# Kernel optimization log

Measured on AMD Instinct MI355X. Metric: run time of the kernel, lower is better.

## Reference

```python
import jax, jax.numpy as jnp
import numpy as np

NEG = -1e30  # log-space -inf surrogate (safe for logaddexp in fp32)


def _ctc_mean_loss(y_true, y_pred):
    """tf.nn.ctc_loss with blank_index=-1, logit_length=T, label_length=#nonzero.

    y_true: [B, L] int labels, 0 = padding, packed at the front.
    y_pred: [B, T, C] logits. blank = C-1. Returns mean NLL over batch.
    """
    B, L = y_true.shape
    T, C = y_pred.shape[1], y_pred.shape[2]
    blank = C - 1
    S = 2 * L + 1  # extended label length (blanks interleaved)

    label_length = jnp.sum((y_true != 0).astype(jnp.int32), axis=1)  # [B]
    logp = jax.nn.log_softmax(y_pred, axis=-1)  # [B, T, C]

    # Extended sequence: blank, l1, blank, l2, ..., blank
    ext = jnp.full((B, S), blank, dtype=jnp.int32)
    ext = ext.at[:, 1::2].set(y_true.astype(jnp.int32))  # [B, S]

    # skip transition (s-2 -> s) allowed only at odd s>=3 when labels differ
    skip_ok = jnp.zeros((B, S), dtype=bool)
    skip_ok = skip_ok.at[:, 3::2].set(y_true[:, 1:] != y_true[:, :-1])

    # alpha_0
    alpha0 = jnp.full((B, S), NEG, dtype=logp.dtype)
    alpha0 = alpha0.at[:, 0].set(logp[:, 0, blank])
    alpha0 = alpha0.at[:, 1].set(
        jnp.take_along_axis(logp[:, 0, :], ext[:, 1:2], axis=1)[:, 0])

    def step(alpha, logp_t):  # alpha [B,S], logp_t [B,C]
        s1 = jnp.pad(alpha, ((0, 0), (1, 0)), constant_values=NEG)[:, :-1]
        s2 = jnp.pad(alpha, ((0, 0), (2, 0)), constant_values=NEG)[:, :-2]
        comb = jnp.logaddexp(jnp.logaddexp(alpha, s1),
                             jnp.where(skip_ok, s2, NEG))
        emit = jnp.take_along_axis(logp_t, ext, axis=1)  # [B,S]
        return comb + emit, None

    alphaT, _ = jax.lax.scan(step, alpha0, jnp.swapaxes(logp, 0, 1)[1:])

    # P(labels) = alpha_T[2l] + alpha_T[2l-1]  (last blank / last label)
    l = label_length
    idx = jnp.stack([2 * l, 2 * l - 1], axis=1)  # [B,2], l>=1 by construction
    fin = jnp.take_along_axis(alphaT, idx, axis=1)
    loss = -jnp.logaddexp(fin[:, 0], fin[:, 1])  # [B]
    return jnp.mean(loss)


def setup_inputs() -> dict:
    key = jax.random.key(0)
    k1, k2, k3 = jax.random.split(key, 3)
    B, T, L, C = 256, 512, 128, 128
    lengths = jax.random.randint(k1, (B,), L // 2, L + 1)  # labels per example
    vals = jax.random.randint(k2, (B, L), 1, C - 1)  # classes 1..C-2 (blank=C-1)
    mask = jnp.arange(L)[None, :] < lengths[:, None]
    y_true = jnp.where(mask, vals, 0).astype(jnp.int32)
    y_pred = jax.random.normal(k3, (B, T, C), dtype=jnp.float32)
    return {"y_true": y_true, "y_pred": y_pred}


def reference(y_true, y_pred):
    return _ctc_mean_loss(y_true, y_pred)
```

## Files before the change

kernel.cpp:

```cpp
#include <hip/hip_runtime.h>
#include <hip/hip_fp16.h>

#define LN2D 0.6931471805599453094172321

typedef float v2f __attribute__((ext_vector_type(2)));

__device__ __forceinline__ float shr1(float v, float fill) {
    return __int_as_float(__builtin_amdgcn_update_dpp(
        __float_as_int(fill), __float_as_int(v), 0x138 , 0xF, 0xF, false));
}
__device__ __forceinline__ float shl1(float v, float fill) {
    return __int_as_float(__builtin_amdgcn_update_dpp(
        __float_as_int(fill), __float_as_int(v), 0x130 , 0xF, 0xF, false));
}

__device__ __forceinline__ float wave_sum63(float x) {
    int t;
    t = __builtin_amdgcn_update_dpp(0, __float_as_int(x), 0x111, 0xF, 0xF, true);
    x += __int_as_float(t);
    t = __builtin_amdgcn_update_dpp(0, __float_as_int(x), 0x112, 0xF, 0xF, true);
    x += __int_as_float(t);
    t = __builtin_amdgcn_update_dpp(0, __float_as_int(x), 0x114, 0xF, 0xF, true);
    x += __int_as_float(t);
    t = __builtin_amdgcn_update_dpp(0, __float_as_int(x), 0x118, 0xF, 0xF, true);
    x += __int_as_float(t);
    t = __builtin_amdgcn_update_dpp(0, __float_as_int(x), 0x142, 0xA, 0xF, true);
    x += __int_as_float(t);
    t = __builtin_amdgcn_update_dpp(0, __float_as_int(x), 0x143, 0xC, 0xF, true);
    x += __int_as_float(t);
    return x;
}

__device__ __forceinline__ float wave_max63(float x) {
    int iv = __float_as_int(x); int t;
    t = __builtin_amdgcn_update_dpp(iv, iv, 0x111, 0xF, 0xF, false);
    x = fmaxf(x, __int_as_float(t)); iv = __float_as_int(x);
    t = __builtin_amdgcn_update_dpp(iv, iv, 0x112, 0xF, 0xF, false);
    x = fmaxf(x, __int_as_float(t)); iv = __float_as_int(x);
    t = __builtin_amdgcn_update_dpp(iv, iv, 0x114, 0xF, 0xF, false);
    x = fmaxf(x, __int_as_float(t)); iv = __float_as_int(x);
    t = __builtin_amdgcn_update_dpp(iv, iv, 0x118, 0xF, 0xF, false);
    x = fmaxf(x, __int_as_float(t)); iv = __float_as_int(x);
    t = __builtin_amdgcn_update_dpp(iv, iv, 0x142, 0xA, 0xF, false);
    x = fmaxf(x, __int_as_float(t)); iv = __float_as_int(x);
    t = __builtin_amdgcn_update_dpp(iv, iv, 0x143, 0xC, 0xF, false);
    x = fmaxf(x, __int_as_float(t));
    return x;
}

__device__ __forceinline__ float rdl63(float v) {
    return __int_as_float(__builtin_amdgcn_readlane(__float_as_int(v), 63));
}

__device__ __forceinline__ int pk_bf16(float a, float b) {
    unsigned ua = __float_as_uint(a), ub = __float_as_uint(b);
    ua = (ua + 0x7FFFu + ((ua >> 16) & 1u)) >> 16;
    ub = (ub + 0x7FFFu + ((ub >> 16) & 1u)) & 0xFFFF0000u;
    return (int)(ua | ub);
}

#define VSTRIDE 260

__global__ __launch_bounds__(256) void ctc_half(const int* __restrict__ yt,
                                                const float* __restrict__ yp,
                                                float* __restrict__ V,
                                                int* __restrict__ E,
                                                float* __restrict__ accW) {
    constexpr int L = 128;
    const int bh   = blockIdx.x;
    const int b    = bh >> 1, h = bh & 1;
    const int w    = threadIdx.x >> 6;
    const int lane = threadIdx.x & 63;

    __shared__ int g[256][64];

    const int2 cc = *reinterpret_cast<const int2*>(yt + b * L + 2 * lane);
    const int c1 = cc.x, c3 = cc.y;
    const int sl1 = c1 >> 1, sh1v = (c1 & 1) << 4;
    const int sl3 = c3 >> 1, sh3v = (c3 & 1) << 4;

    float acc = 0.0f;
    const float* src = yp + ((size_t)b * 512 + h * 256 + w * 64) * 128 + lane * 2;
    v2f A8[8], B8[8];

#define ISSUE8(d_, p_)                                                         \
    asm volatile(                                                              \
        "global_load_dwordx2 %0, %8, off\n\t"                                  \
        "global_load_dwordx2 %1, %8, off offset:512\n\t"                       \
        "global_load_dwordx2 %2, %8, off offset:1024\n\t"                      \
        "global_load_dwordx2 %3, %8, off offset:1536\n\t"                      \
        "global_load_dwordx2 %4, %8, off offset:2048\n\t"                      \
        "global_load_dwordx2 %5, %8, off offset:2560\n\t"                      \
        "global_load_dwordx2 %6, %8, off offset:3072\n\t"                      \
        "global_load_dwordx2 %7, %8, off offset:3584"                          \
        : "=&v"(d_[0]), "=&v"(d_[1]), "=&v"(d_[2]), "=&v"(d_[3]),              \
          "=&v"(d_[4]), "=&v"(d_[5]), "=&v"(d_[6]), "=&v"(d_[7])               \
        : "v"(p_)                                                              \
        : "memory");

#define WAITN(n_)                                                              \
    {                                                                          \
        asm volatile("s_waitcnt vmcnt(" #n_ ")" ::: "memory");                 \
        __builtin_amdgcn_sched_barrier(0);                                     \
    }

#define PROC8(buf_, rb_)                                                       \
    {                                                                          \
        _Pragma("unroll")                                                      \
        for (int i = 0; i < 8; ++i) {                                          \
            const float vx = buf_[i].x, vy = buf_[i].y;                        \
            const float sall = rdl63(wave_sum63(__expf(vx) + __expf(vy)));     \
            const float xbv  = rdl63(vy);                \
            acc += __logf(sall) - xbv;                                         \
            const __half2 hh = __floats2half2_rn(vx, vy);                      \
            const int hb = __builtin_bit_cast(int, hh);                        \
            const int q1 = __shfl(hb, sl1, 64);                                \
            const int q3 = __shfl(hb, sl3, 64);                                \
            const float x1 = __half2float(__builtin_bit_cast(__half, (unsigned short)(q1 >> sh1v))); \
            const float x3 = __half2float(__builtin_bit_cast(__half, (unsigned short)(q3 >> sh3v))); \
            g[w * 64 + (rb_) + i][lane] =                                      \
                pk_bf16(__expf(x1 - xbv), __expf(x3 - xbv));                   \
        }                                                                      \
    }

    ISSUE8(A8, src)
    ISSUE8(B8, src + 8 * 128)
    WAITN(8)  PROC8(A8, 0)   ISSUE8(A8, src + 16 * 128)
    WAITN(8)  PROC8(B8, 8)   ISSUE8(B8, src + 24 * 128)
    WAITN(8)  PROC8(A8, 16)  ISSUE8(A8, src + 32 * 128)
    WAITN(8)  PROC8(B8, 24)  ISSUE8(B8, src + 40 * 128)
    WAITN(8)  PROC8(A8, 32)  ISSUE8(A8, src + 48 * 128)
    WAITN(8)  PROC8(B8, 40)  ISSUE8(B8, src + 56 * 128)
    WAITN(8)  PROC8(A8, 48)
    WAITN(0)  PROC8(B8, 56)

    if (lane == 0) accW[bh * 4 + w] = acc;
    __syncthreads();

    if (w == 0) {
        const int cprev = __shfl_up(c3, 1, 64);
        const float sk1 = (lane > 0 && c1 != cprev) ? 1.0f : 0.0f;
        const float sk3 = (c3 != c1) ? 1.0f : 0.0f;
        const float skB3 = shl1(sk1, 0.0f);
        const int llen = __popcll(__ballot(c1 != 0)) + __popcll(__ballot(c3 != 0));

        float o0, o1, o2, o3, o4;
        int   Eacc = 0;
        int   er[8];

#define RENORM()                                                               \
    {                                                                          \
        float mr = fmaxf(fmaxf(fmaxf(o0, o1), fmaxf(o2, o3)), o4);             \
        const float mru = rdl63(wave_max63(mr));                               \
        const int ie = (__float_as_int(mru) >> 23) & 0xFF;                     \
        const float sc = __int_as_float((253 - ie) << 23);                     \
        o0 *= sc; o1 *= sc; o2 *= sc; o3 *= sc; o4 *= sc;                      \
        Eacc += ie - 126;                                                      \
    }

#define FSTEP(bits_, rn_)                                                      \
    {                                                                          \
        const float e1 = __int_as_float((bits_) << 16);                        \
        const float e3 = __int_as_float((bits_) & 0xFFFF0000);                 \
        const float pm = shr1(o3, 0.0f);                                       \
        const float n0 = o0 + pm;                                              \
        const float n1 = (o1 + o0 + sk1 * pm) * e1;                            \
        const float n2 = o2 + o1;                                              \
        const float n3 = (o3 + o2 + sk3 * o1) * e3;                            \
        o4 += o3;                                                              \
        o0 = n0; o1 = n1; o2 = n2; o3 = n3;                                    \
        if (rn_) RENORM();                                                     \
    }

#define BSTEP(bits_, rn_)                                                      \
    {                                                                          \
        const float e1 = __int_as_float((bits_) << 16);                        \
        const float e3 = __int_as_float((bits_) & 0xFFFF0000);                 \
        const float g1 = o1 * e1;                                              \
        const float g3 = o3 * e3;                                              \
        const float pm0 = shl1(o0, o4);          \
        const float pm1 = shl1(g1, 0.0f);        \
        const float n0 = o0 + g1;                                              \
        const float n1 = g1 + o2 + sk3 * g3;                                   \
        const float n2 = o2 + g3;                                              \
        const float n3 = g3 + pm0 + skB3 * pm1;                                \
        o0 = n0; o1 = n1; o2 = n2; o3 = n3;                                    \
        if (rn_) RENORM();                                                     \
    }

        if (h == 0) {
            #pragma unroll
            for (int i = 0; i < 8; ++i) er[i] = g[i][lane];
            {
                const float e10 = __int_as_float(er[0] << 16);
                o0 = (lane == 0) ? 1.0f : 0.0f;
                o1 = (lane == 0) ? e10 : 0.0f;
                o2 = 0.0f; o3 = 0.0f; o4 = 0.0f;
            }
            er[0] = g[8][lane];
            #pragma unroll
            for (int t = 1; t < 8; ++t) { FSTEP(er[t], false); er[t] = g[t + 8][lane]; }
            #pragma unroll
            for (int tb = 8; tb < 248; tb += 8) {
                #pragma unroll
                for (int j = 0; j < 8; ++j) {
                    FSTEP(er[j], ((tb + j) & 31) == 0);
                    er[j] = g[tb + j + 8][lane];
                }
            }
            #pragma unroll
            for (int t = 248; t < 256; ++t) FSTEP(er[t & 7], false);
        } else {
            #pragma unroll
            for (int i = 0; i < 8; ++i) er[i] = g[255 - i][lane];
            const int sA = 2 * llen, sB = 2 * llen - 1;
            o0 = (4 * lane + 0 == sA) ? 1.0f : 0.0f;
            o1 = (4 * lane + 1 == sB) ? 1.0f : 0.0f;
            o2 = (4 * lane + 2 == sA) ? 1.0f : 0.0f;
            o3 = (4 * lane + 3 == sB) ? 1.0f : 0.0f;
            o4 = (llen == 128 && lane == 63) ? 1.0f : 0.0f;
            #pragma unroll
            for (int kb = 0; kb < 248; kb += 8) {
                #pragma unroll
                for (int j = 0; j < 8; ++j) {
                    const int r = 255 - (kb + j);
                    BSTEP(er[j], (r & 31) == 0);
                    er[j] = g[r - 8][lane];
                }
            }
            #pragma unroll
            for (int k = 248; k < 256; ++k) BSTEP(er[k & 7], ((255 - k) & 31) == 0);
        }

        float* Vh = V + (size_t)bh * VSTRIDE;
        Vh[4 * lane + 0] = o0; Vh[4 * lane + 1] = o1;
        Vh[4 * lane + 2] = o2; Vh[4 * lane + 3] = o3;
        if (lane == 63) Vh[256] = o4;
        if (lane == 0)  E[bh] = Eacc;
#undef BSTEP
#undef FSTEP
#undef RENORM
    }
#undef PROC8
#undef WAITN
#undef ISSUE8
}

__global__ __launch_bounds__(64) void combine(const float* __restrict__ V,
                                              const int* __restrict__ E,
                                              const float* __restrict__ accW,
                                              float* __restrict__ loss) {
    const int b = blockIdx.x, lane = threadIdx.x;
    const float* Vf = V + (size_t)(2 * b) * VSTRIDE;
    const float* Vb = Vf + VSTRIDE;
    const float4 a = *reinterpret_cast<const float4*>(Vf + 4 * lane);
    const float4 c = *reinterpret_cast<const float4*>(Vb + 4 * lane);
    double p = (double)a.x * (double)c.x + (double)a.y * (double)c.y
             + (double)a.z * (double)c.z + (double)a.w * (double)c.w;
    if (lane == 63) p += (double)Vf[256] * (double)Vb[256];
    #pragma unroll
    for (int off = 32; off > 0; off >>= 1) p += __shfl_xor(p, off, 64);
    if (lane == 0) {
        float ls = 0.0f;
        #pragma unroll
        for (int j = 0; j < 8; ++j) ls += accW[8 * b + j];
        const double lg = log(p) + (double)(E[2 * b] + E[2 * b + 1]) * LN2D - (double)ls;
        loss[b] = -(float)lg;
    }
}

__global__ __launch_bounds__(256) void finalize(const float* __restrict__ loss,
                                                float* __restrict__ out) {
    __shared__ float red[256];
    const int tid = threadIdx.x;
    red[tid] = loss[tid];
    __syncthreads();
    for (int off = 128; off > 0; off >>= 1) {
        if (tid < off) red[tid] += red[tid + off];
        __syncthreads();
    }
    if (tid == 0) out[0] = red[0] * (1.0f / 256.0f);
}

extern "C" void kernel_launch(void* const* d_in, const int* in_sizes, int n_in,
                              void* d_out, int out_size, void* d_ws, size_t ws_size,
                              hipStream_t stream) {
    constexpr int B = 256;
    const int*   y_true = (const int*)d_in[0];
    const float* y_pred = (const float*)d_in[1];
    float* out = (float*)d_out;

    float* V    = (float*)d_ws;
    int*   E    = (int*)(V + 512 * VSTRIDE);
    float* accW = (float*)(E + 512);
    float* loss = accW + 2048;

    ctc_half<<<B * 2, 256, 0, stream>>>(y_true, y_pred, V, E, accW);
    combine<<<B, 64, 0, stream>>>(V, E, accW, loss);
    finalize<<<1, 256, 0, stream>>>(loss, out);
}
```

Baseline: 40.80 us.

## Use 512-thread blocks, fp8-like emission storage, and row-wise logsumexp pass

Doubles the threads per half-sequence block so each wave preprocesses 32 timesteps instead of 64, which shortens the load/exp prologue before the serial recursion. Emission ratios are stored as 8-bit truncated fp16 values, halving the LDS footprint and write traffic. The per-timestep wave-wide exp sum is replaced by a separate pass in which each lane pair reduces one row with float4 loads, removing DPP reductions from the main loop. The 8-bit emissions reduce precision in the CTC recursion and may affect accuracy, and the row pass rereads the logits from global memory.

```diff
diff --git a/kernel.cpp b/kernel.cpp
--- a/kernel.cpp
+++ b/kernel.cpp
@@ -52,16 +52,23 @@
     return __int_as_float(__builtin_amdgcn_readlane(__float_as_int(v), 63));
 }
 
-__device__ __forceinline__ int pk_bf16(float a, float b) {
-    unsigned ua = __float_as_uint(a), ub = __float_as_uint(b);
-    ua = (ua + 0x7FFFu + ((ua >> 16) & 1u)) >> 16;
-    ub = (ub + 0x7FFFu + ((ub >> 16) & 1u)) & 0xFFFF0000u;
-    return (int)(ua | ub);
+__device__ __forceinline__ unsigned short pk_fp8(float a, float b) {
+    const unsigned short ha = __builtin_bit_cast(unsigned short, __float2half_rn(a));
+    const unsigned short hb = __builtin_bit_cast(unsigned short, __float2half_rn(b));
+    const unsigned ua = ((unsigned)ha + 0x80u) >> 8;
+    const unsigned ub = (((unsigned)hb + 0x80u) >> 8) << 8;
+    return (unsigned short)(ua | ub);
+}
+__device__ __forceinline__ float dec_lo(unsigned short u) {
+    return __half2float(__builtin_bit_cast(__half, (unsigned short)((u & 0xFFu) << 8)));
+}
+__device__ __forceinline__ float dec_hi(unsigned short u) {
+    return __half2float(__builtin_bit_cast(__half, (unsigned short)(u & 0xFF00u)));
 }
 
 #define VSTRIDE 260
 
-__global__ __launch_bounds__(256) void ctc_half(const int* __restrict__ yt,
+__global__ __launch_bounds__(512) void ctc_half(const int* __restrict__ yt,
                                                 const float* __restrict__ yp,
                                                 float* __restrict__ V,
                                                 int* __restrict__ E,
@@ -72,15 +79,15 @@
     const int w    = threadIdx.x >> 6;
     const int lane = threadIdx.x & 63;
 
-    __shared__ int g[256][64];
+    __shared__ unsigned short g[256][64];
 
     const int2 cc = *reinterpret_cast<const int2*>(yt + b * L + 2 * lane);
     const int c1 = cc.x, c3 = cc.y;
     const int sl1 = c1 >> 1, sh1v = (c1 & 1) << 4;
     const int sl3 = c3 >> 1, sh3v = (c3 & 1) << 4;
 
-    float acc = 0.0f;
-    const float* src = yp + ((size_t)b * 512 + h * 256 + w * 64) * 128 + lane * 2;
+    float xbsum = 0.0f;
+    const float* src = yp + ((size_t)b * 512 + h * 256 + w * 32) * 128 + lane * 2;
     v2f A8[8], B8[8];
 
 #define ISSUE8(d_, p_)                                                         \
@@ -109,17 +116,15 @@
         _Pragma("unroll")                                                      \
         for (int i = 0; i < 8; ++i) {                                          \
             const float vx = buf_[i].x, vy = buf_[i].y;                        \
-            const float sall = rdl63(wave_sum63(__expf(vx) + __expf(vy)));     \
-            const float xbv  = rdl63(vy);                \
-            acc += __logf(sall) - xbv;                                         \
+            const float xbv = rdl63(vy);                 \
+            xbsum += xbv;                                                      \
             const __half2 hh = __floats2half2_rn(vx, vy);                      \
             const int hb = __builtin_bit_cast(int, hh);                        \
             const int q1 = __shfl(hb, sl1, 64);                                \
             const int q3 = __shfl(hb, sl3, 64);                                \
             const float x1 = __half2float(__builtin_bit_cast(__half, (unsigned short)(q1 >> sh1v))); \
             const float x3 = __half2float(__builtin_bit_cast(__half, (unsigned short)(q3 >> sh3v))); \
-            g[w * 64 + (rb_) + i][lane] =                                      \
-                pk_bf16(__expf(x1 - xbv), __expf(x3 - xbv));                   \
+            g[w * 32 + (rb_) + i][lane] = pk_fp8(__expf(x1 - xbv), __expf(x3 - xbv)); \
         }                                                                      \
     }
 
@@ -127,14 +132,23 @@
     ISSUE8(B8, src + 8 * 128)
     WAITN(8)  PROC8(A8, 0)   ISSUE8(A8, src + 16 * 128)
     WAITN(8)  PROC8(B8, 8)   ISSUE8(B8, src + 24 * 128)
-    WAITN(8)  PROC8(A8, 16)  ISSUE8(A8, src + 32 * 128)
-    WAITN(8)  PROC8(B8, 24)  ISSUE8(B8, src + 40 * 128)
-    WAITN(8)  PROC8(A8, 32)  ISSUE8(A8, src + 48 * 128)
-    WAITN(8)  PROC8(B8, 40)  ISSUE8(B8, src + 56 * 128)
-    WAITN(8)  PROC8(A8, 48)
-    WAITN(0)  PROC8(B8, 56)
-
-    if (lane == 0) accW[bh * 4 + w] = acc;
+    WAITN(8)  PROC8(A8, 16)
+    WAITN(0)  PROC8(B8, 24)
+
+    {
+        const int lr = lane & 31, hf = lane >> 5;
+        const float* pb = yp + ((size_t)b * 512 + h * 256 + w * 32 + lr) * 128 + hf * 64;
+        float s = 0.0f;
+        #pragma unroll
+        for (int j = 0; j < 16; ++j) {
+            const float4 f = *reinterpret_cast<const float4*>(pb + 4 * j);
+            s += (__expf(f.x) + __expf(f.y)) + (__expf(f.z) + __expf(f.w));
+        }
+        const float full = s + __shfl_xor(s, 32, 64);
+        const float lg = __logf(full);
+        const float tot = rdl63(wave_sum63((lane < 32) ? lg : 0.0f));
+        if (lane == 0) accW[bh * 8 + w] = tot - xbsum;
+    }
     __syncthreads();
 
     if (w == 0) {
@@ -146,7 +160,7 @@
 
         float o0, o1, o2, o3, o4;
         int   Eacc = 0;
-        int   er[8];
+        unsigned short er[8];
 
 #define RENORM()                                                               \
     {                                                                          \
@@ -160,8 +174,8 @@
 
 #define FSTEP(bits_, rn_)                                                      \
     {                                                                          \
-        const float e1 = __int_as_float((bits_) << 16);                        \
-        const float e3 = __int_as_float((bits_) & 0xFFFF0000);                 \
+        const float e1 = dec_lo(bits_);                                        \
+        const float e3 = dec_hi(bits_);                                        \
         const float pm = shr1(o3, 0.0f);                                       \
         const float n0 = o0 + pm;                                              \
         const float n1 = (o1 + o0 + sk1 * pm) * e1;                            \
@@ -174,8 +188,8 @@
 
 #define BSTEP(bits_, rn_)                                                      \
     {                                                                          \
-        const float e1 = __int_as_float((bits_) << 16);                        \
-        const float e3 = __int_as_float((bits_) & 0xFFFF0000);                 \
+        const float e1 = dec_lo(bits_);                                        \
+        const float e3 = dec_hi(bits_);                                        \
         const float g1 = o1 * e1;                                              \
         const float g3 = o3 * e3;                                              \
         const float pm0 = shl1(o0, o4);          \
@@ -192,7 +206,7 @@
             #pragma unroll
             for (int i = 0; i < 8; ++i) er[i] = g[i][lane];
             {
-                const float e10 = __int_as_float(er[0] << 16);
+                const float e10 = dec_lo(er[0]);
                 o0 = (lane == 0) ? 1.0f : 0.0f;
                 o1 = (lane == 0) ? e10 : 0.0f;
                 o2 = 0.0f; o3 = 0.0f; o4 = 0.0f;
@@ -263,7 +277,7 @@
     if (lane == 0) {
         float ls = 0.0f;
         #pragma unroll
-        for (int j = 0; j < 8; ++j) ls += accW[8 * b + j];
+        for (int j = 0; j < 16; ++j) ls += accW[16 * b + j];
         const double lg = log(p) + (double)(E[2 * b] + E[2 * b + 1]) * LN2D - (double)ls;
         loss[b] = -(float)lg;
     }
@@ -293,9 +307,9 @@
     float* V    = (float*)d_ws;
     int*   E    = (int*)(V + 512 * VSTRIDE);
     float* accW = (float*)(E + 512);
-    float* loss = accW + 2048;
-
-    ctc_half<<<B * 2, 256, 0, stream>>>(y_true, y_pred, V, E, accW);
+    float* loss = accW + 512 * 8;
+
+    ctc_half<<<B * 2, 512, 0, stream>>>(y_true, y_pred, V, E, accW);
     combine<<<B, 64, 0, stream>>>(V, E, accW, loss);
     finalize<<<1, 256, 0, stream>>>(loss, out);
 }
```

After: 41.42 us. Within noise of the previous version (+1.5%).
